# Performance work log

Measured on AMD Instinct MI355X. Metric: run time of the kernel, lower is better.

The kernel has to match this reference:

```python
import jax, jax.numpy as jnp
import numpy as np

N_EMBEDDING = 512
EMBEDDING_DIM = 64
COMMITMENT_COST = 0.25


def setup_inputs() -> dict:
    key = jax.random.key(0)
    k1, k2 = jax.random.split(key)
    inputs = jax.random.normal(k1, (64, 32, 32, EMBEDDING_DIM), dtype=jnp.float32)
    context = jnp.zeros((1,), dtype=jnp.float32)  # unused by the module
    # variance_scaling(1.0, 'fan_in', 'uniform') on shape (D, K): fan_in = D
    limit = np.sqrt(3.0 / EMBEDDING_DIM)
    embeddings = jax.random.uniform(
        k2, (EMBEDDING_DIM, N_EMBEDDING), dtype=jnp.float32,
        minval=-limit, maxval=limit)
    return {"inputs": inputs, "context": context, "embeddings": embeddings}


def reference(inputs, context, embeddings):
    D, K = embeddings.shape
    flat = inputs.reshape(-1, D)  # [N, D]
    distances = (
        jnp.sum(jnp.square(flat), axis=1, keepdims=True)
        - 2.0 * jnp.matmul(flat, embeddings)
        + jnp.sum(jnp.square(embeddings), axis=0, keepdims=True)
    )
    encoding_indices_flat = jnp.argmax(-distances, axis=1)  # [N]
    encodings = jax.nn.one_hot(encoding_indices_flat, K, dtype=distances.dtype)
    encoding_indices = encoding_indices_flat.reshape(inputs.shape[:-1])
    # gather codebook rows: embeddings.T is [K, D]
    quantized = embeddings.T[encoding_indices]  # [B, H, W, D]

    e_latent_loss = jnp.mean(jnp.square(jax.lax.stop_gradient(quantized) - inputs))
    q_latent_loss = jnp.mean(jnp.square(quantized - jax.lax.stop_gradient(inputs)))
    loss = q_latent_loss + COMMITMENT_COST * e_latent_loss

    # straight-through estimator
    quantized = inputs + jax.lax.stop_gradient(quantized - inputs)

    avg_probs = jnp.mean(encodings, axis=0)
    perplexity = jnp.exp(-jnp.sum(avg_probs * jnp.log(avg_probs + 1e-10)))
    return (quantized, loss, perplexity, encodings, encoding_indices, distances)
```

## Files before the change

kernel.cpp:

```cpp
#include <hip/hip_runtime.h>


#define NROWS 65536
#define DIM 64
#define KCODES 512
#define ROWS_PER_BLOCK 128
#define NBLOCKS (NROWS / ROWS_PER_BLOCK)
#define RPT 8

#define QUANT_OFF 0ull
#define LOSS_OFF  4194304ull
#define PERP_OFF  4194305ull
#define ENC_OFF   4194306ull
#define IDX_OFF   37748738ull
#define DIST_OFF  37814274ull

typedef float f32x4 __attribute__((ext_vector_type(4)));

__global__ __launch_bounds__(64) void vq_transpose(
    const float* __restrict__ emb, float* __restrict__ et)
{
    const int t = blockIdx.x * 64 + threadIdx.x;
    f32x4* et4 = (f32x4*)et;
#pragma unroll
    for (int dq = 0; dq < 16; ++dq) {
        f32x4 v;
        v.x = emb[(dq * 4 + 0) * KCODES + t];
        v.y = emb[(dq * 4 + 1) * KCODES + t];
        v.z = emb[(dq * 4 + 2) * KCODES + t];
        v.w = emb[(dq * 4 + 3) * KCODES + t];
        et4[t * 16 + dq] = v;
    }
}

__global__ __launch_bounds__(512, 4) void vq_main(
    const float* __restrict__ inp, const float* __restrict__ emb,
    const float* __restrict__ et,
    float* __restrict__ out, int* __restrict__ hist,
    float* __restrict__ loss_part)
{
    __shared__ f32x4 s_X[ROWS_PER_BLOCK * 16];
    __shared__ float s_sumx2[ROWS_PER_BLOCK];
    __shared__ float s_loss[8];

    const int tid  = threadIdx.x;
    const int w    = tid >> 6;
    const int lane = tid & 63;
    const int rbase = blockIdx.x * ROWS_PER_BLOCK;

    {
        const f32x4* inp4 = (const f32x4*)inp;
#pragma unroll
        for (int i = 0; i < 4; ++i)
            s_X[i * 512 + tid] = inp4[(size_t)blockIdx.x * 2048 + i * 512 + tid];
    }
    __syncthreads();

    {
        const int row_l = w * 16 + (lane >> 2);
        const int q = lane & 3;
        float p = 0.f;
#pragma unroll
        for (int j = 0; j < 4; ++j) {
            const f32x4 v = s_X[row_l * 16 + q * 4 + j];
            p = fmaf(v.x, v.x, p); p = fmaf(v.y, v.y, p);
            p = fmaf(v.z, v.z, p); p = fmaf(v.w, v.w, p);
        }
        p += __shfl_xor(p, 1);
        p += __shfl_xor(p, 2);
        if (q == 0) s_sumx2[row_l] = p;
    }

    f32x4 sume2_0 = {0.f, 0.f, 0.f, 0.f};
    f32x4 sume2_1 = {0.f, 0.f, 0.f, 0.f};
    float loss_acc = 0.f;

    const float* ebase = emb + lane * 4;
    const f32x4* et4 = (const f32x4*)et;

#pragma unroll 1
    for (int g = 0; g < 2; ++g) {
        const int rl0 = w * 16 + g * RPT;

        f32x4 acc[RPT][2];
#pragma unroll
        for (int r = 0; r < RPT; ++r) {
            acc[r][0] = (f32x4){0.f, 0.f, 0.f, 0.f};
            acc[r][1] = (f32x4){0.f, 0.f, 0.f, 0.f};
        }

#pragma unroll 1
        for (int dq = 0; dq < 16; ++dq) {
            f32x4 e0[4], e1[4];
#pragma unroll
            for (int sub = 0; sub < 4; ++sub) {
                e0[sub] = *(const f32x4*)(ebase + (dq * 4 + sub) * KCODES);
                e1[sub] = *(const f32x4*)(ebase + (dq * 4 + sub) * KCODES + 256);
            }
            if (g == 0) {
#pragma unroll
                for (int sub = 0; sub < 4; ++sub) {
                    sume2_0 = sume2_0 + e0[sub] * e0[sub];
                    sume2_1 = sume2_1 + e1[sub] * e1[sub];
                }
            }
#pragma unroll
            for (int r = 0; r < RPT; ++r) {
                const f32x4 xv = s_X[(rl0 + r) * 16 + dq];
                acc[r][0] = acc[r][0] + xv.x * e0[0];
                acc[r][1] = acc[r][1] + xv.x * e1[0];
                acc[r][0] = acc[r][0] + xv.y * e0[1];
                acc[r][1] = acc[r][1] + xv.y * e1[1];
                acc[r][0] = acc[r][0] + xv.z * e0[2];
                acc[r][1] = acc[r][1] + xv.z * e1[2];
                acc[r][0] = acc[r][0] + xv.w * e0[3];
                acc[r][1] = acc[r][1] + xv.w * e1[3];
            }
        }

#pragma unroll
        for (int r = 0; r < RPT; ++r) {
            const int row = rbase + rl0 + r;
            const float sx2 = s_sumx2[rl0 + r];

            const f32x4 dd0 = (sume2_0 + sx2) + (-2.f) * acc[r][0];
            const f32x4 dd1 = (sume2_1 + sx2) + (-2.f) * acc[r][1];

            f32x4* dp = (f32x4*)(out + DIST_OFF) + (size_t)row * 128;
            __builtin_nontemporal_store(dd0, dp + lane);
            __builtin_nontemporal_store(dd1, dp + 64 + lane);

            float bd = fminf(fminf(fminf(dd0.x, dd0.y), fminf(dd0.z, dd0.w)),
                             fminf(fminf(dd1.x, dd1.y), fminf(dd1.z, dd1.w)));
            const int kb = lane * 4;
            int ck = 0x7fffffff;
            if (dd1.w == bd) ck = 256 + kb + 3;
            if (dd1.z == bd) ck = 256 + kb + 2;
            if (dd1.y == bd) ck = 256 + kb + 1;
            if (dd1.x == bd) ck = 256 + kb + 0;
            if (dd0.w == bd) ck = kb + 3;
            if (dd0.z == bd) ck = kb + 2;
            if (dd0.y == bd) ck = kb + 1;
            if (dd0.x == bd) ck = kb + 0;

            float fd = bd;
#pragma unroll
            for (int off = 32; off; off >>= 1)
                fd = fminf(fd, __shfl_xor(fd, off));
            int c2 = (bd == fd) ? ck : 0x7fffffff;
#pragma unroll
            for (int off = 32; off; off >>= 1) {
                const int ok = __shfl_xor(c2, off);
                c2 = ok < c2 ? ok : c2;
            }

            f32x4* ep = (f32x4*)(out + ENC_OFF) + (size_t)row * 128;
            const int cq = c2 >> 2;
            f32x4 v0 = {0.f, 0.f, 0.f, 0.f};
            f32x4 v1 = {0.f, 0.f, 0.f, 0.f};
            if (cq == lane) {
                v0.x = (c2 & 3) == 0 ? 1.f : 0.f;
                v0.y = (c2 & 3) == 1 ? 1.f : 0.f;
                v0.z = (c2 & 3) == 2 ? 1.f : 0.f;
                v0.w = (c2 & 3) == 3 ? 1.f : 0.f;
            }
            if (cq == 64 + lane) {
                v1.x = (c2 & 3) == 0 ? 1.f : 0.f;
                v1.y = (c2 & 3) == 1 ? 1.f : 0.f;
                v1.z = (c2 & 3) == 2 ? 1.f : 0.f;
                v1.w = (c2 & 3) == 3 ? 1.f : 0.f;
            }
            __builtin_nontemporal_store(v0, ep + lane);
            __builtin_nontemporal_store(v1, ep + 64 + lane);

            if (lane < 16) {
                const f32x4 q = et4[c2 * 16 + lane];
                ((f32x4*)(out + QUANT_OFF + (size_t)row * DIM))[lane] = q;
            }

            if (lane == 0) {
                out[IDX_OFF + row] = (float)c2;
                atomicAdd(&hist[c2], 1);
                loss_acc += fd;
            }
        }
    }

    if (lane == 0) s_loss[w] = loss_acc;
    __syncthreads();
    if (tid == 0) {
        float s = 0.f;
#pragma unroll
        for (int i = 0; i < 8; ++i) s += s_loss[i];
        loss_part[blockIdx.x] = s;
    }
}

__global__ __launch_bounds__(512) void vq_final(
    const int* __restrict__ hist, const float* __restrict__ loss_part,
    float* __restrict__ out)
{
    __shared__ float s_red[8];
    __shared__ float s_red2[8];
    const int tid = threadIdx.x;
    const int w = tid >> 6, lane = tid & 63;

    float p = (float)hist[tid] * (1.f / 65536.f);
    float t = p * logf(p + 1e-10f);
    float l = loss_part[tid];
#pragma unroll
    for (int off = 32; off; off >>= 1) {
        t += __shfl_xor(t, off);
        l += __shfl_xor(l, off);
    }
    if (lane == 0) { s_red[w] = t; s_red2[w] = l; }
    __syncthreads();
    if (tid == 0) {
        float s = 0.f, ls = 0.f;
#pragma unroll
        for (int i = 0; i < 8; ++i) { s += s_red[i]; ls += s_red2[i]; }
        out[PERP_OFF] = expf(-s);
        out[LOSS_OFF] = ls * (1.25f / 4194304.f);
    }
}

extern "C" void kernel_launch(void* const* d_in, const int* in_sizes, int n_in,
                              void* d_out, int out_size, void* d_ws, size_t ws_size,
                              hipStream_t stream) {
    const float* inp = (const float*)d_in[0];
    const float* emb = (const float*)d_in[2];
    float* out = (float*)d_out;
    int*   hist      = (int*)d_ws;
    float* loss_part = (float*)((char*)d_ws + 2048);
    float* et        = (float*)((char*)d_ws + 8192);

    (void)hipMemsetAsync(d_ws, 0, 2048, stream);
    vq_transpose<<<dim3(8), dim3(64), 0, stream>>>(emb, et);
    vq_main<<<dim3(NBLOCKS), dim3(512), 0, stream>>>(
        inp, emb, et, out, hist, loss_part);
    vq_final<<<dim3(1), dim3(512), 0, stream>>>(hist, loss_part, out);
}
```

Before: 104.6 us.

## Stage full codebook in LDS and halve rows per block

Each block now copies the whole 64x512 codebook (128 KB) into shared memory and computes distances from LDS instead of reading embedding rows from global memory for every dq step. Rows per block drop from 128 to 64, so each warp handles one group of 8 rows, and there are twice as many blocks. The final reduction is updated to sum 1024 loss partials. The cost is a 128 KB LDS copy per block before any compute, which limits each CU to about one block and cuts occupancy. It also leaves the load unoverlapped with compute in a kernel dominated by output writes.

```diff
diff --git a/kernel.cpp b/kernel.cpp
--- a/kernel.cpp
+++ b/kernel.cpp
@@ -4,9 +4,9 @@
 #define NROWS 65536
 #define DIM 64
 #define KCODES 512
-#define ROWS_PER_BLOCK 128
+#define ROWS_PER_BLOCK 64
 #define NBLOCKS (NROWS / ROWS_PER_BLOCK)
-#define RPT 8
+#define RPW 8
 
 #define QUANT_OFF 0ull
 #define LOSS_OFF  4194304ull
@@ -33,12 +33,13 @@
     }
 }
 
-__global__ __launch_bounds__(512, 4) void vq_main(
+__global__ __launch_bounds__(512, 2) void vq_main(
     const float* __restrict__ inp, const float* __restrict__ emb,
     const float* __restrict__ et,
     float* __restrict__ out, int* __restrict__ hist,
     float* __restrict__ loss_part)
 {
+    __shared__ f32x4 s_E[16 * KCODES];
     __shared__ f32x4 s_X[ROWS_PER_BLOCK * 16];
     __shared__ float s_sumx2[ROWS_PER_BLOCK];
     __shared__ float s_loss[8];
@@ -47,27 +48,34 @@
     const int w    = tid >> 6;
     const int lane = tid & 63;
     const int rbase = blockIdx.x * ROWS_PER_BLOCK;
+    const int rl0  = w * RPW;
 
     {
-        const f32x4* inp4 = (const f32x4*)inp;
-#pragma unroll
-        for (int i = 0; i < 4; ++i)
-            s_X[i * 512 + tid] = inp4[(size_t)blockIdx.x * 2048 + i * 512 + tid];
+        const f32x4* e4 = (const f32x4*)emb;
+#pragma unroll
+        for (int i = 0; i < 16; ++i)
+            s_E[i * 512 + tid] = e4[i * 512 + tid];
+    }
+    {
+        const f32x4* inp4 = (const f32x4*)inp + (size_t)blockIdx.x * 1024;
+        s_X[tid]       = inp4[tid];
+        s_X[512 + tid] = inp4[512 + tid];
     }
     __syncthreads();
 
     {
-        const int row_l = w * 16 + (lane >> 2);
-        const int q = lane & 3;
+        const int row_l = w * RPW + (lane >> 3);
+        const int q = lane & 7;
+        const f32x4 a = s_X[row_l * 16 + q * 2 + 0];
+        const f32x4 b = s_X[row_l * 16 + q * 2 + 1];
         float p = 0.f;
-#pragma unroll
-        for (int j = 0; j < 4; ++j) {
-            const f32x4 v = s_X[row_l * 16 + q * 4 + j];
-            p = fmaf(v.x, v.x, p); p = fmaf(v.y, v.y, p);
-            p = fmaf(v.z, v.z, p); p = fmaf(v.w, v.w, p);
-        }
+        p = fmaf(a.x, a.x, p); p = fmaf(a.y, a.y, p);
+        p = fmaf(a.z, a.z, p); p = fmaf(a.w, a.w, p);
+        p = fmaf(b.x, b.x, p); p = fmaf(b.y, b.y, p);
+        p = fmaf(b.z, b.z, p); p = fmaf(b.w, b.w, p);
         p += __shfl_xor(p, 1);
         p += __shfl_xor(p, 2);
+        p += __shfl_xor(p, 4);
         if (q == 0) s_sumx2[row_l] = p;
     }
 
@@ -75,114 +83,106 @@
     f32x4 sume2_1 = {0.f, 0.f, 0.f, 0.f};
     float loss_acc = 0.f;
 
-    const float* ebase = emb + lane * 4;
+    f32x4 acc[RPW][2];
+#pragma unroll
+    for (int r = 0; r < RPW; ++r) {
+        acc[r][0] = (f32x4){0.f, 0.f, 0.f, 0.f};
+        acc[r][1] = (f32x4){0.f, 0.f, 0.f, 0.f};
+    }
+
+#pragma unroll 1
+    for (int dq = 0; dq < 16; ++dq) {
+        f32x4 e0[4], e1[4];
+#pragma unroll
+        for (int sub = 0; sub < 4; ++sub) {
+            e0[sub] = s_E[(dq * 4 + sub) * 128 + lane];
+            e1[sub] = s_E[(dq * 4 + sub) * 128 + 64 + lane];
+        }
+#pragma unroll
+        for (int sub = 0; sub < 4; ++sub) {
+            sume2_0 = sume2_0 + e0[sub] * e0[sub];
+            sume2_1 = sume2_1 + e1[sub] * e1[sub];
+        }
+#pragma unroll
+        for (int r = 0; r < RPW; ++r) {
+            const f32x4 xv = s_X[(rl0 + r) * 16 + dq];
+            acc[r][0] = acc[r][0] + xv.x * e0[0];
+            acc[r][1] = acc[r][1] + xv.x * e1[0];
+            acc[r][0] = acc[r][0] + xv.y * e0[1];
+            acc[r][1] = acc[r][1] + xv.y * e1[1];
+            acc[r][0] = acc[r][0] + xv.z * e0[2];
+            acc[r][1] = acc[r][1] + xv.z * e1[2];
+            acc[r][0] = acc[r][0] + xv.w * e0[3];
+            acc[r][1] = acc[r][1] + xv.w * e1[3];
+        }
+    }
+
     const f32x4* et4 = (const f32x4*)et;
 
-#pragma unroll 1
-    for (int g = 0; g < 2; ++g) {
-        const int rl0 = w * 16 + g * RPT;
-
-        f32x4 acc[RPT][2];
-#pragma unroll
-        for (int r = 0; r < RPT; ++r) {
-            acc[r][0] = (f32x4){0.f, 0.f, 0.f, 0.f};
-            acc[r][1] = (f32x4){0.f, 0.f, 0.f, 0.f};
-        }
-
-#pragma unroll 1
-        for (int dq = 0; dq < 16; ++dq) {
-            f32x4 e0[4], e1[4];
-#pragma unroll
-            for (int sub = 0; sub < 4; ++sub) {
-                e0[sub] = *(const f32x4*)(ebase + (dq * 4 + sub) * KCODES);
-                e1[sub] = *(const f32x4*)(ebase + (dq * 4 + sub) * KCODES + 256);
-            }
-            if (g == 0) {
-#pragma unroll
-                for (int sub = 0; sub < 4; ++sub) {
-                    sume2_0 = sume2_0 + e0[sub] * e0[sub];
-                    sume2_1 = sume2_1 + e1[sub] * e1[sub];
-                }
-            }
-#pragma unroll
-            for (int r = 0; r < RPT; ++r) {
-                const f32x4 xv = s_X[(rl0 + r) * 16 + dq];
-                acc[r][0] = acc[r][0] + xv.x * e0[0];
-                acc[r][1] = acc[r][1] + xv.x * e1[0];
-                acc[r][0] = acc[r][0] + xv.y * e0[1];
-                acc[r][1] = acc[r][1] + xv.y * e1[1];
-                acc[r][0] = acc[r][0] + xv.z * e0[2];
-                acc[r][1] = acc[r][1] + xv.z * e1[2];
-                acc[r][0] = acc[r][0] + xv.w * e0[3];
-                acc[r][1] = acc[r][1] + xv.w * e1[3];
-            }
-        }
-
-#pragma unroll
-        for (int r = 0; r < RPT; ++r) {
-            const int row = rbase + rl0 + r;
-            const float sx2 = s_sumx2[rl0 + r];
-
-            const f32x4 dd0 = (sume2_0 + sx2) + (-2.f) * acc[r][0];
-            const f32x4 dd1 = (sume2_1 + sx2) + (-2.f) * acc[r][1];
-
-            f32x4* dp = (f32x4*)(out + DIST_OFF) + (size_t)row * 128;
-            __builtin_nontemporal_store(dd0, dp + lane);
-            __builtin_nontemporal_store(dd1, dp + 64 + lane);
-
-            float bd = fminf(fminf(fminf(dd0.x, dd0.y), fminf(dd0.z, dd0.w)),
-                             fminf(fminf(dd1.x, dd1.y), fminf(dd1.z, dd1.w)));
-            const int kb = lane * 4;
-            int ck = 0x7fffffff;
-            if (dd1.w == bd) ck = 256 + kb + 3;
-            if (dd1.z == bd) ck = 256 + kb + 2;
-            if (dd1.y == bd) ck = 256 + kb + 1;
-            if (dd1.x == bd) ck = 256 + kb + 0;
-            if (dd0.w == bd) ck = kb + 3;
-            if (dd0.z == bd) ck = kb + 2;
-            if (dd0.y == bd) ck = kb + 1;
-            if (dd0.x == bd) ck = kb + 0;
-
-            float fd = bd;
-#pragma unroll
-            for (int off = 32; off; off >>= 1)
-                fd = fminf(fd, __shfl_xor(fd, off));
-            int c2 = (bd == fd) ? ck : 0x7fffffff;
-#pragma unroll
-            for (int off = 32; off; off >>= 1) {
-                const int ok = __shfl_xor(c2, off);
-                c2 = ok < c2 ? ok : c2;
-            }
-
-            f32x4* ep = (f32x4*)(out + ENC_OFF) + (size_t)row * 128;
-            const int cq = c2 >> 2;
-            f32x4 v0 = {0.f, 0.f, 0.f, 0.f};
-            f32x4 v1 = {0.f, 0.f, 0.f, 0.f};
-            if (cq == lane) {
-                v0.x = (c2 & 3) == 0 ? 1.f : 0.f;
-                v0.y = (c2 & 3) == 1 ? 1.f : 0.f;
-                v0.z = (c2 & 3) == 2 ? 1.f : 0.f;
-                v0.w = (c2 & 3) == 3 ? 1.f : 0.f;
-            }
-            if (cq == 64 + lane) {
-                v1.x = (c2 & 3) == 0 ? 1.f : 0.f;
-                v1.y = (c2 & 3) == 1 ? 1.f : 0.f;
-                v1.z = (c2 & 3) == 2 ? 1.f : 0.f;
-                v1.w = (c2 & 3) == 3 ? 1.f : 0.f;
-            }
-            __builtin_nontemporal_store(v0, ep + lane);
-            __builtin_nontemporal_store(v1, ep + 64 + lane);
-
-            if (lane < 16) {
-                const f32x4 q = et4[c2 * 16 + lane];
-                ((f32x4*)(out + QUANT_OFF + (size_t)row * DIM))[lane] = q;
-            }
-
-            if (lane == 0) {
-                out[IDX_OFF + row] = (float)c2;
-                atomicAdd(&hist[c2], 1);
-                loss_acc += fd;
-            }
+#pragma unroll
+    for (int r = 0; r < RPW; ++r) {
+        const int row = rbase + rl0 + r;
+        const float sx2 = s_sumx2[rl0 + r];
+
+        const f32x4 dd0 = (sume2_0 + sx2) + (-2.f) * acc[r][0];
+        const f32x4 dd1 = (sume2_1 + sx2) + (-2.f) * acc[r][1];
+
+        f32x4* dp = (f32x4*)(out + DIST_OFF) + (size_t)row * 128;
+        __builtin_nontemporal_store(dd0, dp + lane);
+        __builtin_nontemporal_store(dd1, dp + 64 + lane);
+
+        float bd = fminf(fminf(fminf(dd0.x, dd0.y), fminf(dd0.z, dd0.w)),
+                         fminf(fminf(dd1.x, dd1.y), fminf(dd1.z, dd1.w)));
+        const int kb = lane * 4;
+        int ck = 0x7fffffff;
+        if (dd1.w == bd) ck = 256 + kb + 3;
+        if (dd1.z == bd) ck = 256 + kb + 2;
+        if (dd1.y == bd) ck = 256 + kb + 1;
+        if (dd1.x == bd) ck = 256 + kb + 0;
+        if (dd0.w == bd) ck = kb + 3;
+        if (dd0.z == bd) ck = kb + 2;
+        if (dd0.y == bd) ck = kb + 1;
+        if (dd0.x == bd) ck = kb + 0;
+
+        float fd = bd;
+#pragma unroll
+        for (int off = 32; off; off >>= 1)
+            fd = fminf(fd, __shfl_xor(fd, off));
+        int c2 = (bd == fd) ? ck : 0x7fffffff;
+#pragma unroll
+        for (int off = 32; off; off >>= 1) {
+            const int ok = __shfl_xor(c2, off);
+            c2 = ok < c2 ? ok : c2;
+        }
+
+        f32x4* ep = (f32x4*)(out + ENC_OFF) + (size_t)row * 128;
+        const int cq = c2 >> 2;
+        f32x4 v0 = {0.f, 0.f, 0.f, 0.f};
+        f32x4 v1 = {0.f, 0.f, 0.f, 0.f};
+        if (cq == lane) {
+            v0.x = (c2 & 3) == 0 ? 1.f : 0.f;
+            v0.y = (c2 & 3) == 1 ? 1.f : 0.f;
+            v0.z = (c2 & 3) == 2 ? 1.f : 0.f;
+            v0.w = (c2 & 3) == 3 ? 1.f : 0.f;
+        }
+        if (cq == 64 + lane) {
+            v1.x = (c2 & 3) == 0 ? 1.f : 0.f;
+            v1.y = (c2 & 3) == 1 ? 1.f : 0.f;
+            v1.z = (c2 & 3) == 2 ? 1.f : 0.f;
+            v1.w = (c2 & 3) == 3 ? 1.f : 0.f;
+        }
+        __builtin_nontemporal_store(v0, ep + lane);
+        __builtin_nontemporal_store(v1, ep + 64 + lane);
+
+        if (lane < 16) {
+            const f32x4 q = et4[c2 * 16 + lane];
+            ((f32x4*)(out + QUANT_OFF + (size_t)row * DIM))[lane] = q;
+        }
+
+        if (lane == 0) {
+            out[IDX_OFF + row] = (float)c2;
+            atomicAdd(&hist[c2], 1);
+            loss_acc += fd;
         }
     }
 
@@ -207,7 +207,7 @@
 
     float p = (float)hist[tid] * (1.f / 65536.f);
     float t = p * logf(p + 1e-10f);
-    float l = loss_part[tid];
+    float l = loss_part[tid] + loss_part[tid + 512];
 #pragma unroll
     for (int off = 32; off; off >>= 1) {
         t += __shfl_xor(t, off);
```

New measurement: 112.6 us. +7.7%, slower.
